# Performance work log

Hardware: AMD Instinct MI355X
Metric: run time of the kernel (lower is better)

The kernel has to match this reference:

```python
import jax, jax.numpy as jnp
import numpy as np

N_NODES = 50000
N_EDGES = 1600000
F_IN = 128
NUM_CLASSES = 40


def _gat_conv(x, src, dst, W, a_src, a_dst, b, concat):
    # x: [N, Fin], W: [Fin, H*C], a_src/a_dst: [H, C], b: [H*C] or [C]
    H, C = a_src.shape
    N = x.shape[0]
    h = (x @ W).reshape(N, H, C)                       # [N,H,C]
    al_s = jnp.einsum('nhc,hc->nh', h, a_src)          # [N,H]
    al_d = jnp.einsum('nhc,hc->nh', h, a_dst)          # [N,H]
    e = jax.nn.leaky_relu(al_s[src] + al_d[dst], 0.2)  # [E,H]
    # segment softmax over destination nodes
    m = jax.ops.segment_max(e, dst, num_segments=N)    # [N,H]
    ex = jnp.exp(e - m[dst])
    s = jax.ops.segment_sum(ex, dst, num_segments=N)   # [N,H]
    alpha = ex / s[dst]                                # [E,H]
    out = jax.ops.segment_sum(h[src] * alpha[:, :, None], dst, num_segments=N)  # [N,H,C]
    if concat:
        return out.reshape(N, H * C) + b
    return out.mean(axis=1) + b


def setup_inputs() -> dict:
    key = jax.random.key(0)
    ks = jax.random.split(key, 12)
    s = 0.1
    inp = {
        'x': jax.random.normal(ks[0], (N_NODES, F_IN), jnp.float32),
        'edge_index': jax.random.randint(ks[1], (2, N_EDGES), 0, N_NODES, jnp.int64),
        # conv1: 128 -> 16, heads=4, concat
        'W1': jax.random.normal(ks[2], (F_IN, 4 * 16), jnp.float32) * s,
        'a1s': jax.random.normal(ks[3], (4, 16), jnp.float32) * s,
        'a1d': jax.random.normal(ks[4], (4, 16), jnp.float32) * s,
        'b1': jnp.zeros((4 * 16,), jnp.float32),
        # conv2: 64 -> 16, heads=4, concat
        'W2': jax.random.normal(ks[5], (64, 4 * 16), jnp.float32) * s,
        'a2s': jax.random.normal(ks[6], (4, 16), jnp.float32) * s,
        'a2d': jax.random.normal(ks[7], (4, 16), jnp.float32) * s,
        'b2': jnp.zeros((4 * 16,), jnp.float32),
        # conv3: 64 -> num_classes, heads=6, mean
        'W3': jax.random.normal(ks[8], (64, 6 * NUM_CLASSES), jnp.float32) * s,
        'a3s': jax.random.normal(ks[9], (6, NUM_CLASSES), jnp.float32) * s,
        'a3d': jax.random.normal(ks[10], (6, NUM_CLASSES), jnp.float32) * s,
        'b3': jnp.zeros((NUM_CLASSES,), jnp.float32),
    }
    return inp


def reference(x, edge_index, W1, a1s, a1d, b1, W2, a2s, a2d, b2, W3, a3s, a3d, b3):
    N = x.shape[0]
    loop = jnp.arange(N, dtype=edge_index.dtype)
    src = jnp.concatenate([edge_index[0], loop])  # add_self_loops=True (PyG default)
    dst = jnp.concatenate([edge_index[1], loop])
    h = jax.nn.elu(_gat_conv(x, src, dst, W1, a1s, a1d, b1, concat=True))
    h = jax.nn.elu(_gat_conv(h, src, dst, W2, a2s, a2d, b2, concat=True))
    h = jax.nn.elu(_gat_conv(h, src, dst, W3, a3s, a3d, b3, concat=False))
    return jax.nn.log_softmax(h, axis=1)
```

## Files before the change

kernel.cpp:

```cpp
#include <hip/hip_runtime.h>
#include <math.h>

#define N_NODES 50000
#define N_EDGES 1600000
#define NB      391
#define CHUNK   8192
#define NCHUNK  196
#define LOG2E   1.44269504088896340736f

typedef __attribute__((ext_vector_type(2))) float v2f;
typedef __attribute__((ext_vector_type(4))) float f32x4;
typedef __attribute__((ext_vector_type(8))) __bf16 bf16x8;

__device__ __forceinline__ float lrelu02(float x) { return fmaxf(x, 0.2f * x); }
__device__ __forceinline__ float elu1(float x)    { return x > 0.f ? x : __expf(x) - 1.f; }
__device__ __forceinline__ float exp2_fast(float x) {
    float r; asm("v_exp_f32 %0, %1" : "=v"(r) : "v"(x)); return r;
}

__device__ __forceinline__ unsigned short f2bf(float f) {
    unsigned int u = __float_as_uint(f);
    return (unsigned short)((u + 0x7fffu + ((u >> 16) & 1u)) >> 16);
}
__device__ __forceinline__ float bf2f(unsigned short s) {
    return __uint_as_float((unsigned int)s << 16);
}
__device__ __forceinline__ float2 bfp2(unsigned int u) {
    float2 r;
    r.x = __uint_as_float(u << 16);
    r.y = __uint_as_float(u & 0xffff0000u);
    return r;
}

union BF8U { unsigned short u[8]; bf16x8 v; };
__device__ __forceinline__ bf16x8 cvt8(float4 a, float4 b) {
    BF8U r;
    r.u[0] = f2bf(a.x); r.u[1] = f2bf(a.y); r.u[2] = f2bf(a.z); r.u[3] = f2bf(a.w);
    r.u[4] = f2bf(b.x); r.u[5] = f2bf(b.y); r.u[6] = f2bf(b.z); r.u[7] = f2bf(b.w);
    return r.v;
}

template<int FIN>
__global__ __launch_bounds__(256) void gemm_al_kernel(const float* __restrict__ x,
                               const float* __restrict__ W,
                               const float* __restrict__ a_s, const float* __restrict__ a_d,
                               unsigned short* __restrict__ h,
                               float* __restrict__ al_s, float* __restrict__ al_d) {
    constexpr int KS = FIN / 32;
    __shared__ alignas(16) unsigned short Wl[KS * 64 * 32];
    __shared__ alignas(16) unsigned short ot[64][64];
    const int tid = threadIdx.x;
    for (int i = tid; i < FIN * 64; i += 256) {
        int ks = i >> 11;
        int rem = i & 2047;
        int c = rem >> 5, r = rem & 31;
        Wl[i] = f2bf(W[(ks * 32 + r) * 64 + c]);
    }
    __syncthreads();

    const int wv = tid >> 6, l = tid & 63;
    const int m = l & 15, g = l >> 4;
    const int n0 = blockIdx.x * 64;
    int row = n0 + wv * 16 + m;
    if (row > N_NODES - 1) row = N_NODES - 1;
    const float* xr = x + (size_t)row * FIN + g * 8;

    f32x4 acc[4] = {};
#pragma unroll
    for (int ks = 0; ks < KS; ++ks) {
        float4 xa = *(const float4*)(xr + ks * 32);
        float4 xb = *(const float4*)(xr + ks * 32 + 4);
        bf16x8 af = cvt8(xa, xb);
        const unsigned short* wp = &Wl[ks * 2048 + g * 8];
#pragma unroll
        for (int t = 0; t < 4; ++t) {
            bf16x8 bf = *(const bf16x8*)(wp + (t * 16 + m) * 32);
            acc[t] = __builtin_amdgcn_mfma_f32_16x16x32_bf16(af, bf, acc[t], 0, 0, 0);
        }
    }
#pragma unroll
    for (int t = 0; t < 4; ++t)
#pragma unroll
        for (int j = 0; j < 4; ++j)
            ot[wv * 16 + g * 4 + j][t * 16 + m] = f2bf(acc[t][j]);
    __syncthreads();

    int vrows = N_NODES - n0; if (vrows > 64) vrows = 64;
    {
        unsigned int* ph = (unsigned int*)(h + (size_t)n0 * 64);
        for (int i = tid; i < vrows * 32; i += 256) {
            int r = i >> 5, c = i & 31;
            ph[i] = *(const unsigned int*)&ot[r][c * 2];
        }
    }
    {
        int node = tid >> 2, hd = tid & 3;
        if (node < vrows) {
            const float* as = a_s + hd * 16;
            const float* ad = a_d + hd * 16;
            float s1 = 0.f, s2 = 0.f;
#pragma unroll
            for (int c = 0; c < 16; c += 2) {
                unsigned int q = *(const unsigned int*)&ot[node][hd * 16 + c];
                float2 p = bfp2(q);
                s1 = fmaf(p.x, as[c], s1);     s2 = fmaf(p.x, ad[c], s2);
                s1 = fmaf(p.y, as[c + 1], s1); s2 = fmaf(p.y, ad[c + 1], s2);
            }
            al_s[(n0 + node) * 4 + hd] = s1 * LOG2E;
            al_d[(n0 + node) * 4 + hd] = s2 * LOG2E;
        }
    }
}

__global__ __launch_bounds__(256) void gemm80_kernel(const float* __restrict__ x,
                              const float* __restrict__ W,
                              const float* __restrict__ a_s, const float* __restrict__ a_d,
                              unsigned int* __restrict__ h8,
                              float* __restrict__ al_s, float* __restrict__ al_d) {
    __shared__ alignas(16) unsigned short Wl[2 * 80 * 32];
    __shared__ alignas(16) unsigned short ot[64][80];
    const int tid = threadIdx.x;
    const int nb = blockIdx.x / 3, third = blockIdx.x % 3;
    const int cb = third * 80;
    for (int i = tid; i < 2 * 80 * 32; i += 256) {
        int ks = i / 2560;
        int rem = i - ks * 2560;
        int c = rem >> 5, r = rem & 31;
        Wl[i] = f2bf(W[(ks * 32 + r) * 240 + cb + c]);
    }
    __syncthreads();

    const int wv = tid >> 6, l = tid & 63;
    const int m = l & 15, g = l >> 4;
    const int n0 = nb * 64;
    int row = n0 + wv * 16 + m;
    if (row > N_NODES - 1) row = N_NODES - 1;
    const float* xr = x + (size_t)row * 64 + g * 8;

    f32x4 acc[5] = {};
#pragma unroll
    for (int ks = 0; ks < 2; ++ks) {
        float4 xa = *(const float4*)(xr + ks * 32);
        float4 xb = *(const float4*)(xr + ks * 32 + 4);
        bf16x8 af = cvt8(xa, xb);
        const unsigned short* wp = &Wl[ks * 2560 + g * 8];
#pragma unroll
        for (int t = 0; t < 5; ++t) {
            bf16x8 bf = *(const bf16x8*)(wp + (t * 16 + m) * 32);
            acc[t] = __builtin_amdgcn_mfma_f32_16x16x32_bf16(af, bf, acc[t], 0, 0, 0);
        }
    }
#pragma unroll
    for (int t = 0; t < 5; ++t)
#pragma unroll
        for (int j = 0; j < 4; ++j)
            ot[wv * 16 + g * 4 + j][t * 16 + m] = f2bf(acc[t][j]);
    __syncthreads();

    int vrows = N_NODES - n0; if (vrows > 64) vrows = 64;
    {
        for (int i = tid; i < vrows * 20; i += 256) {
            int r = i / 20, c = i - r * 20;
            uint2 q = *(const uint2*)&ot[r][c * 4];
            float2 p0 = bfp2(q.x), p1 = bfp2(q.y);
            int lo = __builtin_amdgcn_cvt_pk_fp8_f32(p0.x, p0.y, 0, false);
            unsigned int packed = (unsigned int)__builtin_amdgcn_cvt_pk_fp8_f32(p1.x, p1.y, lo, true);
            h8[(size_t)(n0 + r) * 64 + cb / 4 + c] = packed;
        }
        if (third == 0) {
            for (int i = tid; i < vrows * 4; i += 256)
                h8[(size_t)(n0 + (i >> 2)) * 64 + 60 + (i & 3)] = 0;
        }
    }
    for (int t = tid; t < vrows * 2; t += 256) {
        int node = t >> 1, hh = t & 1;
        int hd = third * 2 + hh;
        const unsigned short* rp = &ot[node][hh * 40];
        const float* as = a_s + hd * 40;
        const float* ad = a_d + hd * 40;
        float s1 = 0.f, s2 = 0.f;
#pragma unroll
        for (int c = 0; c < 40; c += 2) {
            unsigned int q = *(const unsigned int*)(rp + c);
            float2 p = bfp2(q);
            s1 = fmaf(p.x, as[c], s1);     s2 = fmaf(p.x, ad[c], s2);
            s1 = fmaf(p.y, as[c + 1], s1); s2 = fmaf(p.y, ad[c + 1], s2);
        }
        al_s[(n0 + node) * 6 + hd] = s1 * LOG2E;
        al_d[(n0 + node) * 6 + hd] = s2 * LOG2E;
    }
}

__global__ __launch_bounds__(256) void bcnt_kernel(const int* __restrict__ ei, int* __restrict__ bcnt) {
    __shared__ int hist[NB];
    const int t = threadIdx.x;
    for (int i = t; i < NB; i += 256) hist[i] = 0;
    __syncthreads();
    const int e0 = blockIdx.x * CHUNK;
    int n = N_EDGES - e0; if (n > CHUNK) n = CHUNK;
    const int4* d4 = (const int4*)(ei + N_EDGES) + (e0 >> 2);
    for (int i = t; i < (n >> 2); i += 256) {
        int4 d = d4[i];
        atomicAdd(&hist[d.x >> 7], 1);
        atomicAdd(&hist[d.y >> 7], 1);
        atomicAdd(&hist[d.z >> 7], 1);
        atomicAdd(&hist[d.w >> 7], 1);
    }
    __syncthreads();
    for (int b = t; b < NB; b += 256)
        if (hist[b]) atomicAdd(&bcnt[b], hist[b]);
}

__global__ void scan391_kernel(const int* __restrict__ bcnt, int* __restrict__ bbase,
                               int* __restrict__ bcur) {
    __shared__ int wtot[8];
    int b = threadIdx.x;
    int lane = b & 63, w = b >> 6;
    int v = (b < NB) ? bcnt[b] : 0;
    int sc = v;
#pragma unroll
    for (int off = 1; off < 64; off <<= 1) {
        int u = __shfl_up(sc, off);
        if (lane >= off) sc += u;
    }
    if (lane == 63) wtot[w] = sc;
    __syncthreads();
    int add = 0;
    for (int k = 0; k < w; ++k) add += wtot[k];
    int excl = sc - v + add;
    if (b < NB) { bbase[b] = excl; bcur[b * 16] = excl; }
    if (b == 0) bbase[NB] = N_EDGES;
}

__global__ __launch_bounds__(256) void bucket2_kernel(const int* __restrict__ ei,
                                                      int* __restrict__ bcur,
                                                      unsigned int* __restrict__ stage) {
    __shared__ unsigned int vals[CHUNK];
    __shared__ int hist[NB];
    __shared__ int cnt2[NB];
    __shared__ int gbase[NB];
    const int t = threadIdx.x;
    for (int i = t; i < NB; i += 256) { hist[i] = 0; cnt2[i] = 0; }
    __syncthreads();
    const int e0 = blockIdx.x * CHUNK;
    int n = N_EDGES - e0; if (n > CHUNK) n = CHUNK;
    const int4* s4 = (const int4*)ei + (e0 >> 2);
    const int4* d4 = (const int4*)(ei + N_EDGES) + (e0 >> 2);
    for (int i = t; i < (n >> 2); i += 256) {
        int4 s = s4[i], d = d4[i];
        vals[4 * i + 0] = ((unsigned int)d.x << 16) | (unsigned int)s.x;
        vals[4 * i + 1] = ((unsigned int)d.y << 16) | (unsigned int)s.y;
        vals[4 * i + 2] = ((unsigned int)d.z << 16) | (unsigned int)s.z;
        vals[4 * i + 3] = ((unsigned int)d.w << 16) | (unsigned int)s.w;
        atomicAdd(&hist[d.x >> 7], 1);
        atomicAdd(&hist[d.y >> 7], 1);
        atomicAdd(&hist[d.z >> 7], 1);
        atomicAdd(&hist[d.w >> 7], 1);
    }
    __syncthreads();
    for (int b = t; b < NB; b += 256)
        if (hist[b]) gbase[b] = atomicAdd(&bcur[b * 16], hist[b]);
    __syncthreads();
    for (int i = t; i < n; i += 256) {
        unsigned int v = vals[i];
        int b = v >> 23;
        int r = atomicAdd(&cnt2[b], 1);
        stage[gbase[b] + r] = v & 0x7FFFFFu;
    }
}

__global__ __launch_bounds__(256) void place2_kernel(const unsigned int* __restrict__ stage,
                                                     const int* __restrict__ bbase,
                                                     int* __restrict__ rowptr,
                                                     unsigned short* __restrict__ csr) {
    __shared__ int hist[128];
    __shared__ int cur[128];
    __shared__ int wt[2];
    const int b = blockIdx.x;
    const int n0 = b * 128;
    const int t = threadIdx.x;
    const int base = bbase[b];
    const int endp = bbase[b + 1];
    if (t < 128) hist[t] = 0;
    __syncthreads();
    for (int i = base + t; i < endp; i += 256)
        atomicAdd(&hist[stage[i] >> 16], 1);
    __syncthreads();
    int v = 0, sc = 0;
    if (t < 128) {
        v = hist[t];
        int lane = t & 63, w = t >> 6;
        sc = v;
#pragma unroll
        for (int off = 1; off < 64; off <<= 1) {
            int u = __shfl_up(sc, off);
            if (lane >= off) sc += u;
        }
        if (lane == 63) wt[w] = sc;
    }
    __syncthreads();
    if (t < 128) {
        int add = (t >= 64) ? wt[0] : 0;
        int excl = sc - v + add;
        int n = n0 + t;
        if (n <= N_NODES) rowptr[n] = base + excl;
        cur[t] = base + excl;
    }
    __syncthreads();
    for (int i = base + t; i < endp; i += 256) {
        unsigned int e = stage[i];
        int pos = atomicAdd(&cur[e >> 16], 1);
        csr[pos] = (unsigned short)(e & 0xFFFFu);
    }
}

__global__ void agg64_kernel(const int* __restrict__ rowptr, const unsigned short* __restrict__ csr_src,
                             const float* __restrict__ al_s, const float* __restrict__ al_d,
                             const unsigned short* __restrict__ hb, const float* __restrict__ b,
                             float* __restrict__ xn) {
    const int node = blockIdx.x * 4 + (threadIdx.x >> 6);
    const int lane = threadIdx.x & 63;
    const int eg = lane >> 4;
    const int cl = lane & 15;
    const int c0 = cl * 4;
    const int hd = cl >> 2;
    const float ald = al_d[(unsigned)(node * 4 + hd)];
    const int beg = rowptr[node], end = rowptr[node + 1];
    float denom = 0.f, a0 = 0.f, a1 = 0.f, a2 = 0.f, a3 = 0.f;
    if (eg == 0) {
        float w = exp2_fast(lrelu02(al_s[(unsigned)(node * 4 + hd)] + ald));
        uint2 q = *(const uint2*)(hb + (unsigned)(node * 64 + c0));
        float2 p0 = bfp2(q.x), p1 = bfp2(q.y);
        denom = w;
        a0 = w * p0.x; a1 = w * p0.y; a2 = w * p1.x; a3 = w * p1.y;
    }
    int j = beg + eg;
    for (; j + 12 < end; j += 16) {
        int s0 = csr_src[j], s1 = csr_src[j + 4], s2 = csr_src[j + 8], s3 = csr_src[j + 12];
        uint2 q0 = *(const uint2*)(hb + (unsigned)(s0 * 64 + c0));
        uint2 q1 = *(const uint2*)(hb + (unsigned)(s1 * 64 + c0));
        uint2 q2 = *(const uint2*)(hb + (unsigned)(s2 * 64 + c0));
        uint2 q3 = *(const uint2*)(hb + (unsigned)(s3 * 64 + c0));
        float w0 = exp2_fast(lrelu02(al_s[(unsigned)(s0 * 4 + hd)] + ald));
        float w1 = exp2_fast(lrelu02(al_s[(unsigned)(s1 * 4 + hd)] + ald));
        float w2 = exp2_fast(lrelu02(al_s[(unsigned)(s2 * 4 + hd)] + ald));
        float w3 = exp2_fast(lrelu02(al_s[(unsigned)(s3 * 4 + hd)] + ald));
        denom += (w0 + w1) + (w2 + w3);
        float2 p;
        p = bfp2(q0.x); a0 = fmaf(w0, p.x, a0); a1 = fmaf(w0, p.y, a1);
        p = bfp2(q0.y); a2 = fmaf(w0, p.x, a2); a3 = fmaf(w0, p.y, a3);
        p = bfp2(q1.x); a0 = fmaf(w1, p.x, a0); a1 = fmaf(w1, p.y, a1);
        p = bfp2(q1.y); a2 = fmaf(w1, p.x, a2); a3 = fmaf(w1, p.y, a3);
        p = bfp2(q2.x); a0 = fmaf(w2, p.x, a0); a1 = fmaf(w2, p.y, a1);
        p = bfp2(q2.y); a2 = fmaf(w2, p.x, a2); a3 = fmaf(w2, p.y, a3);
        p = bfp2(q3.x); a0 = fmaf(w3, p.x, a0); a1 = fmaf(w3, p.y, a1);
        p = bfp2(q3.y); a2 = fmaf(w3, p.x, a2); a3 = fmaf(w3, p.y, a3);
    }
    for (; j < end; j += 4) {
        int s0 = csr_src[j];
        uint2 q0 = *(const uint2*)(hb + (unsigned)(s0 * 64 + c0));
        float w0 = exp2_fast(lrelu02(al_s[(unsigned)(s0 * 4 + hd)] + ald));
        denom += w0;
        float2 p;
        p = bfp2(q0.x); a0 = fmaf(w0, p.x, a0); a1 = fmaf(w0, p.y, a1);
        p = bfp2(q0.y); a2 = fmaf(w0, p.x, a2); a3 = fmaf(w0, p.y, a3);
    }
    denom += __shfl_xor(denom, 16); denom += __shfl_xor(denom, 32);
    a0 += __shfl_xor(a0, 16); a0 += __shfl_xor(a0, 32);
    a1 += __shfl_xor(a1, 16); a1 += __shfl_xor(a1, 32);
    a2 += __shfl_xor(a2, 16); a2 += __shfl_xor(a2, 32);
    a3 += __shfl_xor(a3, 16); a3 += __shfl_xor(a3, 32);
    if (lane < 16) {
        float r = 1.f / denom;
        float4 bv = *(const float4*)(b + c0);
        float4 o;
        o.x = elu1(fmaf(a0, r, bv.x));
        o.y = elu1(fmaf(a1, r, bv.y));
        o.z = elu1(fmaf(a2, r, bv.z));
        o.w = elu1(fmaf(a3, r, bv.w));
        *(float4*)(xn + (unsigned)(node * 64 + c0)) = o;
    }
}

__global__ void agg240_kernel(const int* __restrict__ rowptr, const unsigned short* __restrict__ csr_src,
                              const float* __restrict__ al_s, const float* __restrict__ al_d,
                              const unsigned int* __restrict__ h8, const float* __restrict__ b3,
                              float* __restrict__ y) {
    __shared__ float sh[4][240];
    const int wv_id = threadIdx.x >> 6;
    const int node = blockIdx.x * 4 + wv_id;
    const int lane = threadIdx.x & 63;
    const int eg = lane >> 5;
    const int cl = lane & 31;
    const int u0 = cl * 2;
    int hd = cl / 5; if (hd > 5) hd = 5;
    const float ald = al_d[(unsigned)(node * 6 + hd)];
    const int beg = rowptr[node], end = rowptr[node + 1];
    float denom = 0.f;
    float acc[8] = {0.f, 0.f, 0.f, 0.f, 0.f, 0.f, 0.f, 0.f};
    auto acc8 = [&](uint2 q, float w) {
        v2f p0 = __builtin_amdgcn_cvt_pk_f32_fp8((int)q.x, false);
        v2f p1 = __builtin_amdgcn_cvt_pk_f32_fp8((int)q.x, true);
        v2f p2 = __builtin_amdgcn_cvt_pk_f32_fp8((int)q.y, false);
        v2f p3 = __builtin_amdgcn_cvt_pk_f32_fp8((int)q.y, true);
        acc[0] = fmaf(w, p0.x, acc[0]); acc[1] = fmaf(w, p0.y, acc[1]);
        acc[2] = fmaf(w, p1.x, acc[2]); acc[3] = fmaf(w, p1.y, acc[3]);
        acc[4] = fmaf(w, p2.x, acc[4]); acc[5] = fmaf(w, p2.y, acc[5]);
        acc[6] = fmaf(w, p3.x, acc[6]); acc[7] = fmaf(w, p3.y, acc[7]);
    };
    if (eg == 0) {
        float w = exp2_fast(lrelu02(al_s[(unsigned)(node * 6 + hd)] + ald));
        uint2 q = *(const uint2*)(h8 + (unsigned)(node * 64) + u0);
        denom = w;
        acc8(q, w);
    }
    int j = beg + eg;
    for (; j + 6 < end; j += 8) {
        int s0 = csr_src[j], s1 = csr_src[j + 2], s2 = csr_src[j + 4], s3 = csr_src[j + 6];
        uint2 q0 = *(const uint2*)(h8 + (unsigned)(s0 * 64) + u0);
        uint2 q1 = *(const uint2*)(h8 + (unsigned)(s1 * 64) + u0);
        uint2 q2 = *(const uint2*)(h8 + (unsigned)(s2 * 64) + u0);
        uint2 q3 = *(const uint2*)(h8 + (unsigned)(s3 * 64) + u0);
        float w0 = exp2_fast(lrelu02(al_s[(unsigned)(s0 * 6 + hd)] + ald));
        float w1 = exp2_fast(lrelu02(al_s[(unsigned)(s1 * 6 + hd)] + ald));
        float w2 = exp2_fast(lrelu02(al_s[(unsigned)(s2 * 6 + hd)] + ald));
        float w3 = exp2_fast(lrelu02(al_s[(unsigned)(s3 * 6 + hd)] + ald));
        denom += (w0 + w1) + (w2 + w3);
        acc8(q0, w0); acc8(q1, w1); acc8(q2, w2); acc8(q3, w3);
    }
    for (; j < end; j += 2) {
        int s0 = csr_src[j];
        uint2 q0 = *(const uint2*)(h8 + (unsigned)(s0 * 64) + u0);
        float w0 = exp2_fast(lrelu02(al_s[(unsigned)(s0 * 6 + hd)] + ald));
        denom += w0;
        acc8(q0, w0);
    }
    denom += __shfl_xor(denom, 32);
#pragma unroll
    for (int i = 0; i < 8; ++i) acc[i] += __shfl_xor(acc[i], 32);
    if (eg == 0 && cl < 30) {
        float r = 1.f / denom;
        float* sp = &sh[wv_id][cl * 8];
#pragma unroll
        for (int i = 0; i < 8; ++i) sp[i] = acc[i] * r;
    }
    __syncthreads();
    float v;
    if (lane < 40) {
        const float* p = sh[wv_id];
        float s = 0.f;
#pragma unroll
        for (int hh = 0; hh < 6; ++hh) s += p[hh * 40 + lane];
        v = elu1(s * (1.f / 6.f) + b3[lane]);
    } else {
        v = -INFINITY;
    }
    float m = v;
#pragma unroll
    for (int o = 32; o > 0; o >>= 1) m = fmaxf(m, __shfl_xor(m, o));
    float ex = (lane < 40) ? __expf(v - m) : 0.f;
    float ssum = ex;
#pragma unroll
    for (int o = 32; o > 0; o >>= 1) ssum += __shfl_xor(ssum, o);
    if (lane < 40) y[(size_t)node * 40 + lane] = v - m - __logf(ssum);
}

extern "C" void kernel_launch(void* const* d_in, const int* in_sizes, int n_in,
                              void* d_out, int out_size, void* d_ws, size_t ws_size,
                              hipStream_t stream) {
    const float* x   = (const float*)d_in[0];
    const int*   ei  = (const int*)d_in[1];
    const float* W1  = (const float*)d_in[2];
    const float* a1s = (const float*)d_in[3];
    const float* a1d = (const float*)d_in[4];
    const float* b1  = (const float*)d_in[5];
    const float* W2  = (const float*)d_in[6];
    const float* a2s = (const float*)d_in[7];
    const float* a2d = (const float*)d_in[8];
    const float* b2  = (const float*)d_in[9];
    const float* W3  = (const float*)d_in[10];
    const float* a3s = (const float*)d_in[11];
    const float* a3d = (const float*)d_in[12];
    const float* b3  = (const float*)d_in[13];
    float* y = (float*)d_out;

    float* ws = (float*)d_ws;
    unsigned short* h_bf = (unsigned short*)ws;
    float* x_buf   = ws + 1600000;
    float* al_s    = ws + 4800000;
    float* al_d    = ws + 5100000;
    unsigned int* h8 = (unsigned int*)(ws + 5400000);
    int*   rowptr  = (int*)(ws + 8600000);
    unsigned short* csr_src = (unsigned short*)(ws + 8650008);
    unsigned int* stage = (unsigned int*)(ws + 9450008);
    int*   bcnt    = (int*)(ws + 11050008);
    int*   bbase   = (int*)(ws + 11050400);
    int*   bcur    = (int*)(ws + 11050792);

    hipMemsetAsync(bcnt, 0, NB * sizeof(int), stream);
    bcnt_kernel<<<NCHUNK, 256, 0, stream>>>(ei, bcnt);
    scan391_kernel<<<1, 512, 0, stream>>>(bcnt, bbase, bcur);
    bucket2_kernel<<<NCHUNK, 256, 0, stream>>>(ei, bcur, stage);
    place2_kernel<<<NB, 256, 0, stream>>>(stage, bbase, rowptr, csr_src);

    const int agg_grid = N_NODES / 4;
    const int gemm_gx = (N_NODES + 63) / 64;

    gemm_al_kernel<128><<<gemm_gx, 256, 0, stream>>>(x, W1, a1s, a1d, h_bf, al_s, al_d);
    agg64_kernel<<<agg_grid, 256, 0, stream>>>(rowptr, csr_src, al_s, al_d, h_bf, b1, x_buf);

    gemm_al_kernel<64><<<gemm_gx, 256, 0, stream>>>(x_buf, W2, a2s, a2d, h_bf, al_s, al_d);
    agg64_kernel<<<agg_grid, 256, 0, stream>>>(rowptr, csr_src, al_s, al_d, h_bf, b2, x_buf);

    gemm80_kernel<<<gemm_gx * 3, 256, 0, stream>>>(x_buf, W3, a3s, a3d, h8, al_s, al_d);
    agg240_kernel<<<agg_grid, 256, 0, stream>>>(rowptr, csr_src, al_s, al_d, h8, b3, y);
}
```

Before: 346.8 us.

## Fuse aggregation with next layer's linear transform and attention logits

The layer-1 and layer-2 aggregation kernels now also compute the next layer's projection (x@W), its bf16/fp8 storage and the attention logits, all from shared memory. This removes the separate GEMM kernels and the fp32 x_buf round-trip through global memory. Separate buffers per layer replace the shared ones. In exchange, every aggregation block converts the full W into LDS (up to 64x240 bf16, about 30KB), and the projection runs on scalar FMAs instead of MFMA. The final aggregation's inner loop is also unrolled from 4 to 8 edges per step.

After: 423.5 us. +22.1%, slower.

```diff
diff --git a/kernel.cpp b/kernel.cpp
--- a/kernel.cpp
+++ b/kernel.cpp
@@ -112,85 +112,6 @@
     }
 }
 
-__global__ __launch_bounds__(256) void gemm80_kernel(const float* __restrict__ x,
-                              const float* __restrict__ W,
-                              const float* __restrict__ a_s, const float* __restrict__ a_d,
-                              unsigned int* __restrict__ h8,
-                              float* __restrict__ al_s, float* __restrict__ al_d) {
-    __shared__ alignas(16) unsigned short Wl[2 * 80 * 32];
-    __shared__ alignas(16) unsigned short ot[64][80];
-    const int tid = threadIdx.x;
-    const int nb = blockIdx.x / 3, third = blockIdx.x % 3;
-    const int cb = third * 80;
-    for (int i = tid; i < 2 * 80 * 32; i += 256) {
-        int ks = i / 2560;
-        int rem = i - ks * 2560;
-        int c = rem >> 5, r = rem & 31;
-        Wl[i] = f2bf(W[(ks * 32 + r) * 240 + cb + c]);
-    }
-    __syncthreads();
-
-    const int wv = tid >> 6, l = tid & 63;
-    const int m = l & 15, g = l >> 4;
-    const int n0 = nb * 64;
-    int row = n0 + wv * 16 + m;
-    if (row > N_NODES - 1) row = N_NODES - 1;
-    const float* xr = x + (size_t)row * 64 + g * 8;
-
-    f32x4 acc[5] = {};
-#pragma unroll
-    for (int ks = 0; ks < 2; ++ks) {
-        float4 xa = *(const float4*)(xr + ks * 32);
-        float4 xb = *(const float4*)(xr + ks * 32 + 4);
-        bf16x8 af = cvt8(xa, xb);
-        const unsigned short* wp = &Wl[ks * 2560 + g * 8];
-#pragma unroll
-        for (int t = 0; t < 5; ++t) {
-            bf16x8 bf = *(const bf16x8*)(wp + (t * 16 + m) * 32);
-            acc[t] = __builtin_amdgcn_mfma_f32_16x16x32_bf16(af, bf, acc[t], 0, 0, 0);
-        }
-    }
-#pragma unroll
-    for (int t = 0; t < 5; ++t)
-#pragma unroll
-        for (int j = 0; j < 4; ++j)
-            ot[wv * 16 + g * 4 + j][t * 16 + m] = f2bf(acc[t][j]);
-    __syncthreads();
-
-    int vrows = N_NODES - n0; if (vrows > 64) vrows = 64;
-    {
-        for (int i = tid; i < vrows * 20; i += 256) {
-            int r = i / 20, c = i - r * 20;
-            uint2 q = *(const uint2*)&ot[r][c * 4];
-            float2 p0 = bfp2(q.x), p1 = bfp2(q.y);
-            int lo = __builtin_amdgcn_cvt_pk_fp8_f32(p0.x, p0.y, 0, false);
-            unsigned int packed = (unsigned int)__builtin_amdgcn_cvt_pk_fp8_f32(p1.x, p1.y, lo, true);
-            h8[(size_t)(n0 + r) * 64 + cb / 4 + c] = packed;
-        }
-        if (third == 0) {
-            for (int i = tid; i < vrows * 4; i += 256)
-                h8[(size_t)(n0 + (i >> 2)) * 64 + 60 + (i & 3)] = 0;
-        }
-    }
-    for (int t = tid; t < vrows * 2; t += 256) {
-        int node = t >> 1, hh = t & 1;
-        int hd = third * 2 + hh;
-        const unsigned short* rp = &ot[node][hh * 40];
-        const float* as = a_s + hd * 40;
-        const float* ad = a_d + hd * 40;
-        float s1 = 0.f, s2 = 0.f;
-#pragma unroll
-        for (int c = 0; c < 40; c += 2) {
-            unsigned int q = *(const unsigned int*)(rp + c);
-            float2 p = bfp2(q);
-            s1 = fmaf(p.x, as[c], s1);     s2 = fmaf(p.x, ad[c], s2);
-            s1 = fmaf(p.y, as[c + 1], s1); s2 = fmaf(p.y, ad[c + 1], s2);
-        }
-        al_s[(n0 + node) * 6 + hd] = s1 * LOG2E;
-        al_d[(n0 + node) * 6 + hd] = s2 * LOG2E;
-    }
-}
-
 __global__ __launch_bounds__(256) void bcnt_kernel(const int* __restrict__ ei, int* __restrict__ bcnt) {
     __shared__ int hist[NB];
     const int t = threadIdx.x;
@@ -314,12 +235,14 @@
     }
 }
 
-__global__ void agg64_kernel(const int* __restrict__ rowptr, const unsigned short* __restrict__ csr_src,
-                             const float* __restrict__ al_s, const float* __restrict__ al_d,
-                             const unsigned short* __restrict__ hb, const float* __restrict__ b,
-                             float* __restrict__ xn) {
-    const int node = blockIdx.x * 4 + (threadIdx.x >> 6);
-    const int lane = threadIdx.x & 63;
+
+__device__ __forceinline__ void agg64_core(const int* __restrict__ rowptr,
+                                           const unsigned short* __restrict__ csr_src,
+                                           const float* __restrict__ al_s,
+                                           const float* __restrict__ al_d,
+                                           const unsigned short* __restrict__ hb,
+                                           const float* __restrict__ bias,
+                                           int node, int lane, float sh_o_row[64]) {
     const int eg = lane >> 4;
     const int cl = lane & 15;
     const int c0 = cl * 4;
@@ -372,13 +295,101 @@
     a3 += __shfl_xor(a3, 16); a3 += __shfl_xor(a3, 32);
     if (lane < 16) {
         float r = 1.f / denom;
-        float4 bv = *(const float4*)(b + c0);
-        float4 o;
-        o.x = elu1(fmaf(a0, r, bv.x));
-        o.y = elu1(fmaf(a1, r, bv.y));
-        o.z = elu1(fmaf(a2, r, bv.z));
-        o.w = elu1(fmaf(a3, r, bv.w));
-        *(float4*)(xn + (unsigned)(node * 64 + c0)) = o;
+        float4 bv = *(const float4*)(bias + c0);
+        sh_o_row[c0 + 0] = elu1(fmaf(a0, r, bv.x));
+        sh_o_row[c0 + 1] = elu1(fmaf(a1, r, bv.y));
+        sh_o_row[c0 + 2] = elu1(fmaf(a2, r, bv.z));
+        sh_o_row[c0 + 3] = elu1(fmaf(a3, r, bv.w));
+    }
+}
+
+__global__ __launch_bounds__(256) void agg_mm64_kernel(
+        const int* __restrict__ rowptr, const unsigned short* __restrict__ csr_src,
+        const float* __restrict__ al_s, const float* __restrict__ al_d,
+        const unsigned short* __restrict__ hb, const float* __restrict__ bias,
+        const float* __restrict__ W, const float* __restrict__ as2, const float* __restrict__ ad2,
+        unsigned short* __restrict__ h_out, float* __restrict__ als_o, float* __restrict__ ald_o) {
+    __shared__ alignas(4) unsigned short Wl[64 * 64];
+    __shared__ float sh_o[4][64];
+    const int tid = threadIdx.x;
+    for (int i = tid; i < 4096; i += 256) Wl[i] = f2bf(W[i]);
+    const int wv = tid >> 6, lane = tid & 63;
+    const int node = blockIdx.x * 4 + wv;
+    agg64_core(rowptr, csr_src, al_s, al_d, hb, bias, node, lane, sh_o[wv]);
+    __syncthreads();
+    if (tid < 128) {
+        int nd = tid >> 5, col0 = (tid & 31) * 2;
+        int gn = blockIdx.x * 4 + nd;
+        const float* op = sh_o[nd];
+        float acc0 = 0.f, acc1 = 0.f;
+#pragma unroll 16
+        for (int k = 0; k < 64; ++k) {
+            float ov = op[k];
+            float2 p = bfp2(*(const unsigned int*)&Wl[k * 64 + col0]);
+            acc0 = fmaf(ov, p.x, acc0);
+            acc1 = fmaf(ov, p.y, acc1);
+        }
+        unsigned int packed = (unsigned int)f2bf(acc0) | ((unsigned int)f2bf(acc1) << 16);
+        ((unsigned int*)h_out)[(unsigned)(gn * 32) + (unsigned)(col0 >> 1)] = packed;
+        float ps = acc0 * as2[col0] + acc1 * as2[col0 + 1];
+        float pd = acc0 * ad2[col0] + acc1 * ad2[col0 + 1];
+        ps += __shfl_xor(ps, 1); ps += __shfl_xor(ps, 2); ps += __shfl_xor(ps, 4);
+        pd += __shfl_xor(pd, 1); pd += __shfl_xor(pd, 2); pd += __shfl_xor(pd, 4);
+        if ((tid & 7) == 0) {
+            int hd = (tid & 31) >> 3;
+            als_o[gn * 4 + hd] = ps * LOG2E;
+            ald_o[gn * 4 + hd] = pd * LOG2E;
+        }
+    }
+}
+
+__global__ __launch_bounds__(256) void agg_mm240_kernel(
+        const int* __restrict__ rowptr, const unsigned short* __restrict__ csr_src,
+        const float* __restrict__ al_s, const float* __restrict__ al_d,
+        const unsigned short* __restrict__ hb, const float* __restrict__ bias,
+        const float* __restrict__ W, const float* __restrict__ as3, const float* __restrict__ ad3,
+        unsigned int* __restrict__ h8, float* __restrict__ als_o, float* __restrict__ ald_o) {
+    __shared__ alignas(8) unsigned short Wl[64 * 240];
+    __shared__ float sh_o[4][64];
+    __shared__ float sh_al[4][12];
+    const int tid = threadIdx.x;
+    for (int i = tid; i < 64 * 240; i += 256) Wl[i] = f2bf(W[i]);
+    if (tid < 48) ((float*)sh_al)[tid] = 0.f;
+    const int wv = tid >> 6, lane = tid & 63;
+    const int node = blockIdx.x * 4 + wv;
+    agg64_core(rowptr, csr_src, al_s, al_d, hb, bias, node, lane, sh_o[wv]);
+    __syncthreads();
+    if (tid < 240) {
+        int nd = tid / 60, q = tid - nd * 60, c0 = q * 4;
+        int gn = blockIdx.x * 4 + nd;
+        const float* op = sh_o[nd];
+        float a0 = 0.f, a1 = 0.f, a2 = 0.f, a3 = 0.f;
+#pragma unroll 8
+        for (int k = 0; k < 64; ++k) {
+            float ov = op[k];
+            uint2 wq = *(const uint2*)&Wl[k * 240 + c0];
+            float2 p0 = bfp2(wq.x), p1 = bfp2(wq.y);
+            a0 = fmaf(ov, p0.x, a0); a1 = fmaf(ov, p0.y, a1);
+            a2 = fmaf(ov, p1.x, a2); a3 = fmaf(ov, p1.y, a3);
+        }
+        int lo = __builtin_amdgcn_cvt_pk_fp8_f32(a0, a1, 0, false);
+        unsigned int packed = (unsigned int)__builtin_amdgcn_cvt_pk_fp8_f32(a2, a3, lo, true);
+        h8[(unsigned)(gn * 64 + q)] = packed;
+        int hd = c0 / 40;
+        float ps = a0 * as3[c0] + a1 * as3[c0 + 1] + a2 * as3[c0 + 2] + a3 * as3[c0 + 3];
+        float pd = a0 * ad3[c0] + a1 * ad3[c0 + 1] + a2 * ad3[c0 + 2] + a3 * ad3[c0 + 3];
+        atomicAdd(&sh_al[nd][hd * 2 + 0], ps);
+        atomicAdd(&sh_al[nd][hd * 2 + 1], pd);
+    } else {
+        int t = tid - 240, nd = t >> 2, c = t & 3;
+        h8[(unsigned)((blockIdx.x * 4 + nd) * 64 + 60 + c)] = 0u;
+    }
+    __syncthreads();
+    if (tid < 24) {
+        int nd = tid / 6, hd = tid - nd * 6;
+        int gn = blockIdx.x * 4 + nd;
+        als_o[gn * 6 + hd] = sh_al[nd][hd * 2 + 0] * LOG2E;
+        ald_o[gn * 6 + hd] = sh_al[nd][hd * 2 + 1] * LOG2E;
     }
 }
 
@@ -415,18 +426,18 @@
         acc8(q, w);
     }
     int j = beg + eg;
-    for (; j + 6 < end; j += 8) {
-        int s0 = csr_src[j], s1 = csr_src[j + 2], s2 = csr_src[j + 4], s3 = csr_src[j + 6];
-        uint2 q0 = *(const uint2*)(h8 + (unsigned)(s0 * 64) + u0);
-        uint2 q1 = *(const uint2*)(h8 + (unsigned)(s1 * 64) + u0);
-        uint2 q2 = *(const uint2*)(h8 + (unsigned)(s2 * 64) + u0);
-        uint2 q3 = *(const uint2*)(h8 + (unsigned)(s3 * 64) + u0);
-        float w0 = exp2_fast(lrelu02(al_s[(unsigned)(s0 * 6 + hd)] + ald));
-        float w1 = exp2_fast(lrelu02(al_s[(unsigned)(s1 * 6 + hd)] + ald));
-        float w2 = exp2_fast(lrelu02(al_s[(unsigned)(s2 * 6 + hd)] + ald));
-        float w3 = exp2_fast(lrelu02(al_s[(unsigned)(s3 * 6 + hd)] + ald));
-        denom += (w0 + w1) + (w2 + w3);
-        acc8(q0, w0); acc8(q1, w1); acc8(q2, w2); acc8(q3, w3);
+    for (; j + 14 < end; j += 16) {
+        int s[8];
+#pragma unroll
+        for (int u = 0; u < 8; ++u) s[u] = csr_src[j + 2 * u];
+        uint2 q[8];
+#pragma unroll
+        for (int u = 0; u < 8; ++u) q[u] = *(const uint2*)(h8 + (unsigned)(s[u] * 64) + u0);
+        float w[8];
+#pragma unroll
+        for (int u = 0; u < 8; ++u) w[u] = exp2_fast(lrelu02(al_s[(unsigned)(s[u] * 6 + hd)] + ald));
+#pragma unroll
+        for (int u = 0; u < 8; ++u) { denom += w[u]; acc8(q[u], w[u]); }
     }
     for (; j < end; j += 2) {
         int s0 = csr_src[j];
@@ -485,17 +496,21 @@
     float* y = (float*)d_out;
 
     float* ws = (float*)d_ws;
-    unsigned short* h_bf = (unsigned short*)ws;
-    float* x_buf   = ws + 1600000;
-    float* al_s    = ws + 4800000;
-    float* al_d    = ws + 5100000;
-    unsigned int* h8 = (unsigned int*)(ws + 5400000);
-    int*   rowptr  = (int*)(ws + 8600000);
-    unsigned short* csr_src = (unsigned short*)(ws + 8650008);
-    unsigned int* stage = (unsigned int*)(ws + 9450008);
-    int*   bcnt    = (int*)(ws + 11050008);
-    int*   bbase   = (int*)(ws + 11050400);
-    int*   bcur    = (int*)(ws + 11050792);
+    unsigned short* h1 = (unsigned short*)ws;
+    unsigned short* h2 = (unsigned short*)(ws + 1600000);
+    float* al1_s = ws + 3200000;
+    float* al1_d = ws + 3400000;
+    float* al2_s = ws + 3600000;
+    float* al2_d = ws + 3800000;
+    float* al3_s = ws + 4000000;
+    float* al3_d = ws + 4300000;
+    unsigned int* h8 = (unsigned int*)(ws + 4600000);
+    int* rowptr = (int*)(ws + 7800000);
+    unsigned short* csr_src = (unsigned short*)(ws + 7850008);
+    unsigned int* stage = (unsigned int*)(ws + 8650008);
+    int* bcnt  = (int*)(ws + 10250008);
+    int* bbase = (int*)(ws + 10250400);
+    int* bcur  = (int*)(ws + 10250792);
 
     hipMemsetAsync(bcnt, 0, NB * sizeof(int), stream);
     bcnt_kernel<<<NCHUNK, 256, 0, stream>>>(ei, bcnt);
@@ -506,12 +521,10 @@
     const int agg_grid = N_NODES / 4;
     const int gemm_gx = (N_NODES + 63) / 64;
 
-    gemm_al_kernel<128><<<gemm_gx, 256, 0, stream>>>(x, W1, a1s, a1d, h_bf, al_s, al_d);
-    agg64_kernel<<<agg_grid, 256, 0, stream>>>(rowptr, csr_src, al_s, al_d, h_bf, b1, x_buf);
-
-    gemm_al_kernel<64><<<gemm_gx, 256, 0, stream>>>(x_buf, W2, a2s, a2d, h_bf, al_s, al_d);
-    agg64_kernel<<<agg_grid, 256, 0, stream>>>(rowptr, csr_src, al_s, al_d, h_bf, b2, x_buf);
-
-    gemm80_kernel<<<gemm_gx * 3, 256, 0, stream>>>(x_buf, W3, a3s, a3d, h8, al_s, al_d);
-    agg240_kernel<<<agg_grid, 256, 0, stream>>>(rowptr, csr_src, al_s, al_d, h8, b3, y);
-}
+    gemm_al_kernel<128><<<gemm_gx, 256, 0, stream>>>(x, W1, a1s, a1d, h1, al1_s, al1_d);
+    agg_mm64_kernel<<<agg_grid, 256, 0, stream>>>(rowptr, csr_src, al1_s, al1_d, h1, b1,
+                                                  W2, a2s, a2d, h2, al2_s, al2_d);
+    agg_mm240_kernel<<<agg_grid, 256, 0, stream>>>(rowptr, csr_src, al2_s, al2_d, h2, b2,
+                                                   W3, a3s, a3d, h8, al3_s, al3_d);
+    agg240_kernel<<<agg_grid, 256, 0, stream>>>(rowptr, csr_src, al3_s, al3_d, h8, b3, y);
+}
```
